# Kernel tuning notes

Hardware: AMD Instinct MI355X
Metric: run time of the kernel (lower is better)

## Reference

```python
import jax, jax.numpy as jnp
import numpy as np

B, N, L, D, H, NLAYERS, V = 8, 1024, 16, 256, 4, 2, 32000
DH = D // H  # per-head dim


def setup_inputs() -> dict:
    key = jax.random.key(0)
    ks = jax.random.split(key, 7)
    cfg_adj = jax.random.randint(ks[0], (B, N, N), 0, 2, dtype=jnp.int32)
    cfg_nodes = jax.random.randint(ks[1], (B, N, L), 0, V, dtype=jnp.int32)
    cfg_len = jax.random.randint(ks[2], (B,), 1, N + 1, dtype=jnp.int32)
    emb = jax.random.normal(ks[3], (V, D), jnp.float32) * 0.02
    # xavier-ish scale for per-head projections and attention vectors
    W = jax.random.normal(ks[4], (NLAYERS, H, D, DH), jnp.float32) * np.float32(np.sqrt(2.0 / (D + DH)))
    a_src = jax.random.normal(ks[5], (NLAYERS, H, DH), jnp.float32) * 0.1
    a_dst = jax.random.normal(ks[6], (NLAYERS, H, DH), jnp.float32) * 0.1
    ln_scale = jnp.ones((NLAYERS, D), jnp.float32)
    ln_bias = jnp.zeros((NLAYERS, D), jnp.float32)
    return {"cfg_adj": cfg_adj, "cfg_nodes": cfg_nodes, "cfg_len": cfg_len,
            "emb": emb, "W": W, "a_src": a_src, "a_dst": a_dst,
            "ln_scale": ln_scale, "ln_bias": ln_bias}


def _layer_norm(x, scale, bias, eps=1e-5):
    mu = jnp.mean(x, axis=-1, keepdims=True)
    var = jnp.var(x, axis=-1, keepdims=True)
    return (x - mu) * jax.lax.rsqrt(var + eps) * scale + bias


def reference(cfg_adj, cfg_nodes, cfg_len, emb, W, a_src, a_dst, ln_scale, ln_bias):
    # node features: mean over token embeddings (dropout is identity in eval)
    node_feat = emb[cfg_nodes].mean(axis=2)                       # (B,N,D)
    # add self-loops once (repeated add+clamp in the original is idempotent)
    adj = jnp.minimum(cfg_adj + jnp.eye(N, dtype=cfg_adj.dtype)[None], 1)
    neg_mask = (adj == 0)[:, None]                                # (B,1,N,N)
    h = node_feat
    for l in range(NLAYERS):
        Wh = jnp.einsum('bnd,hdk->bhnk', h, W[l])                 # (B,H,N,DH)
        src = jnp.einsum('bhnk,hk->bhn', Wh, a_src[l])            # (B,H,N)
        dst = jnp.einsum('bhnk,hk->bhn', Wh, a_dst[l])            # (B,H,N)
        e = jax.nn.leaky_relu(src[:, :, :, None] + dst[:, :, None, :], 0.2)
        e = jnp.where(neg_mask, jnp.float32(-1e9), e)             # masked fill
        alpha = jax.nn.softmax(e, axis=-1)                        # (B,H,N,N)
        h_prime = jnp.einsum('bhnm,bhmk->bhnk', alpha, Wh)        # (B,H,N,DH)
        h_cat = jnp.transpose(h_prime, (0, 2, 1, 3)).reshape(B, N, D)
        h = _layer_norm(h + h_cat, ln_scale[l], ln_bias[l])
    return h, cfg_len
```

## Files before the change

kernel.cpp:

```cpp
#include <hip/hip_runtime.h>
#include <math.h>

#define B 8
#define N 1024
#define L 16
#define D 256
#define H 4
#define DH 64
#define NLAYERS 2
#define V 32000

typedef __attribute__((ext_vector_type(8))) short short8;
typedef __attribute__((ext_vector_type(4))) float f32x4;

union U8 { uint4 u; short8 s; };

__device__ inline unsigned short f2bf(float x) {
    unsigned u = __float_as_uint(x);
    u = (u + 0x7fff + ((u >> 16) & 1)) >> 16;
    return (unsigned short)u;
}
__device__ inline float bf2f(unsigned short x) {
    return __uint_as_float(((unsigned)x) << 16);
}


#define PACK_BLK 2048
#define WT_BLK   (NLAYERS * H * 4)
#define PRE_GRID (PACK_BLK + WT_BLK + 1)

__global__ __launch_bounds__(256) void k_pre(const int* __restrict__ adj,
                                             const float* __restrict__ W,
                                             const int* __restrict__ len,
                                             unsigned long long* __restrict__ pack,
                                             unsigned short* __restrict__ WT_sw,
                                             float* __restrict__ out_len) {
    int bid = blockIdx.x;
    int t = threadIdx.x;
    if (bid < PACK_BLK) {
        int row = bid * 4 + (t >> 6);
        int lane = t & 63;
        int n = row & (N - 1);
        const int* arow = adj + (long)row * N;
        unsigned long long* prow = pack + (size_t)row * 16;
        int g16 = lane & 15;
#pragma unroll
        for (int it = 0; it < 4; ++it) {
            int m0 = it * 256 + lane * 4;
            int4 a = *(const int4*)(arow + m0);
            unsigned nib = (unsigned)((a.x != 0) || (m0 == n))
                         | ((unsigned)((a.y != 0) || (m0 + 1 == n)) << 1)
                         | ((unsigned)((a.z != 0) || (m0 + 2 == n)) << 2)
                         | ((unsigned)((a.w != 0) || (m0 + 3 == n)) << 3);
            unsigned long long v = (unsigned long long)nib << (g16 * 4);
            v |= __shfl_xor(v, 1, 64);
            v |= __shfl_xor(v, 2, 64);
            v |= __shfl_xor(v, 4, 64);
            v |= __shfl_xor(v, 8, 64);
            if (g16 == 0) prow[it * 4 + (lane >> 4)] = v;
        }
    } else if (bid < PACK_BLK + WT_BLK) {
        int idx = bid - PACK_BLK;
        int lh = idx >> 2, q = idx & 3;
        const float* Wl = W + (size_t)lh * D * DH;
        int dh = t & 63;
        int d0 = q * 64 + (t >> 6) * 16;
#pragma unroll
        for (int i = 0; i < 16; ++i) {
            int d = d0 + i;
            WT_sw[(((size_t)lh * 8 + (d >> 5)) * 64 + dh) * 32 + (d & 31)] = f2bf(Wl[(size_t)d * DH + dh]);
        }
    } else {
        if (t < B) out_len[t] = (float)len[t];
    }
}

__device__ inline void wh_tile(const unsigned short* __restrict__ hA,
                               const unsigned short* __restrict__ WT_l,
                               const float* __restrict__ asrc_l,
                               const float* __restrict__ adst_l,
                               unsigned short* __restrict__ WhT_out,
                               float* __restrict__ srcv_out,
                               float* __restrict__ dstv_out,
                               int b, int n0, int hh, int lane) {
    int rowLane = lane & 15, quad = lane >> 4;
    int bh = b * H + hh;
    const unsigned short* abase = hA + rowLane * 32 + quad * 8;
    const unsigned short* bbase = WT_l + (size_t)hh * 16384 + rowLane * 32 + quad * 8;
    f32x4 acc[4] = {};
#pragma unroll
    for (int kc = 0; kc < 8; ++kc) {
        short8 af = *(const short8*)(abase + kc * 512);
#pragma unroll
        for (int c = 0; c < 4; ++c) {
            short8 bf = *(const short8*)(bbase + (size_t)kc * 2048 + c * 512);
            acc[c] = __builtin_amdgcn_mfma_f32_16x16x32_bf16(af, bf, acc[c], 0, 0, 0);
        }
    }
    int m0 = n0 + quad * 4;
    float ps[4] = {0.f, 0.f, 0.f, 0.f}, pd[4] = {0.f, 0.f, 0.f, 0.f};
#pragma unroll
    for (int c = 0; c < 4; ++c) {
        int dh = c * 16 + rowLane;
        ushort4 o;
        o.x = f2bf(acc[c][0]); o.y = f2bf(acc[c][1]);
        o.z = f2bf(acc[c][2]); o.w = f2bf(acc[c][3]);
        *(ushort4*)&WhT_out[(((size_t)bh * 32 + (m0 >> 5)) * 64 + dh) * 32 + (m0 & 31)] = o;
        float as = asrc_l[hh * DH + dh];
        float ad = adst_l[hh * DH + dh];
#pragma unroll
        for (int r = 0; r < 4; ++r) { ps[r] += acc[c][r] * as; pd[r] += acc[c][r] * ad; }
    }
#pragma unroll
    for (int off = 1; off < 16; off <<= 1) {
#pragma unroll
        for (int r = 0; r < 4; ++r) {
            ps[r] += __shfl_xor(ps[r], off, 64);
            pd[r] += __shfl_xor(pd[r], off, 64);
        }
    }
    if (rowLane == 0) {
#pragma unroll
        for (int r = 0; r < 4; ++r) {
            srcv_out[bh * N + m0 + r] = ps[r];
            dstv_out[bh * N + m0 + r] = pd[r];
        }
    }
}

__global__ __launch_bounds__(1024) void k_feat(const float* __restrict__ emb,
                                               const int* __restrict__ nodes,
                                               unsigned short* __restrict__ h_sw,
                                               const unsigned short* __restrict__ WT0,
                                               const float* __restrict__ asrc0,
                                               const float* __restrict__ adst0,
                                               unsigned short* __restrict__ WhT0,
                                               float* __restrict__ srcv0,
                                               float* __restrict__ dstv0) {
    __shared__ __align__(16) int nodesLds[256];
    __shared__ __align__(16) unsigned short hA[8 * 16 * 32];
    int tid = threadIdx.x;
    int bt = blockIdx.x;
    int b = bt >> 6, nt = bt & 63, n0 = nt * 16;
    if (tid < 256) nodesLds[tid] = nodes[(size_t)(b * N + n0) * L + tid];
    __syncthreads();
    int w = tid >> 6, lane = tid & 63;
    int d4 = lane * 4;
    const int* np = nodesLds + w * L;
    float4 s = make_float4(0.f, 0.f, 0.f, 0.f);
#pragma unroll
    for (int l = 0; l < L; ++l) {
        float4 v = *(const float4*)&emb[(size_t)np[l] * D + d4];
        s.x += v.x; s.y += v.y; s.z += v.z; s.w += v.w;
    }
    s.x *= (1.0f / L); s.y *= (1.0f / L); s.z *= (1.0f / L); s.w *= (1.0f / L);
    ushort4 o;
    o.x = f2bf(s.x); o.y = f2bf(s.y); o.z = f2bf(s.z); o.w = f2bf(s.w);
    int off = (d4 >> 5) * 512 + w * 32 + (d4 & 31);
    *(ushort4*)&hA[off] = o;
    *(ushort4*)&h_sw[((size_t)(b * 64 + nt) * 8) * 512 + off] = o;
    __syncthreads();
    if (w < 4) wh_tile(hA, WT0, asrc0, adst0, WhT0, srcv0, dstv0, b, n0, w, lane);
}

template <int FINAL>
__global__ __launch_bounds__(256) void k_attn_f(const unsigned long long* __restrict__ pack,
                                                const float* __restrict__ srcv_in,
                                                const float* __restrict__ dstv_in,
                                                const unsigned short* __restrict__ WhT_in,
                                                unsigned short* __restrict__ h_sw,
                                                const float* __restrict__ scale_l,
                                                const float* __restrict__ bias_l,
                                                const unsigned short* __restrict__ WT_next,
                                                const float* __restrict__ asrc_n,
                                                const float* __restrict__ adst_n,
                                                unsigned short* __restrict__ WhT_out,
                                                float* __restrict__ srcv_out,
                                                float* __restrict__ dstv_out,
                                                float* __restrict__ out) {
    __shared__ __align__(16) char smem[25600];
    float* dsts = (float*)smem;
    unsigned long long* packs = (unsigned long long*)(smem + 16384);
    float* xt = (float*)smem;
    unsigned short* hA = (unsigned short*)(smem + 17408);

    int tid = threadIdx.x;
    int bt = blockIdx.x;
    int b = bt >> 6, nt = bt & 63, n0 = nt * 16;
    int w = tid >> 6, lane = tid & 63;
    int rowLane = lane & 15, quad = lane >> 4;
    int bh = b * H + w;

    {
        const float* dv = dstv_in + (size_t)bh * N;
#pragma unroll
        for (int k = 0; k < 4; ++k)
            *(float4*)(dsts + w * 1024 + k * 256 + lane * 4) = *(const float4*)(dv + k * 256 + lane * 4);
        packs[tid] = pack[((size_t)(b * N + n0 + (tid >> 4))) * 16 + (tid & 15)];
    }
    __syncthreads();

    float src = srcv_in[bh * N + n0 + rowLane];
    float mx = src > 0.f ? src : 0.2f * src;
    const unsigned* prow = (const unsigned*)packs + rowLane * 32;
    const unsigned short* wbase = WhT_in + (size_t)bh * 65536 + rowLane * 32 + quad * 8;
    const float* dw = dsts + w * 1024 + quad * 8;

    f32x4 acc[4] = {};
    float sum0 = 0.f, sum1 = 0.f;
    short8 fb[2][4];
#pragma unroll
    for (int c = 0; c < 4; ++c) fb[0][c] = *(const short8*)(wbase + c * 512);
#pragma unroll 2
    for (int t2 = 0; t2 < 32; ++t2) {
        int cb = t2 & 1;
        int t2n = (t2 + 1) & 31;
#pragma unroll
        for (int c = 0; c < 4; ++c)
            fb[cb ^ 1][c] = *(const short8*)(wbase + (size_t)t2n * 2048 + c * 512);
        unsigned bits = (prow[t2] >> (quad * 8)) & 0xffu;
        float4 d0 = *(const float4*)(dw + t2 * 32);
        float4 d1 = *(const float4*)(dw + t2 * 32 + 4);
        float dd[8] = {d0.x, d0.y, d0.z, d0.w, d1.x, d1.y, d1.z, d1.w};
        unsigned pk[4];
#pragma unroll
        for (int j2 = 0; j2 < 4; ++j2) {
            float ea = src + dd[2 * j2];
            float eb = src + dd[2 * j2 + 1];
            ea = ea > 0.f ? ea : 0.2f * ea;
            eb = eb > 0.f ? eb : 0.2f * eb;
            float pa = ((bits >> (2 * j2)) & 1) ? __expf(ea - mx) : 0.f;
            float pb = ((bits >> (2 * j2 + 1)) & 1) ? __expf(eb - mx) : 0.f;
            sum0 += pa; sum1 += pb;
            pk[j2] = (__float_as_uint(pb) & 0xffff0000u) | (__float_as_uint(pa) >> 16);
        }
        U8 u; u.u = make_uint4(pk[0], pk[1], pk[2], pk[3]);
        short8 af = u.s;
        acc[0] = __builtin_amdgcn_mfma_f32_16x16x32_bf16(af, fb[cb][0], acc[0], 0, 0, 0);
        acc[1] = __builtin_amdgcn_mfma_f32_16x16x32_bf16(af, fb[cb][1], acc[1], 0, 0, 0);
        acc[2] = __builtin_amdgcn_mfma_f32_16x16x32_bf16(af, fb[cb][2], acc[2], 0, 0, 0);
        acc[3] = __builtin_amdgcn_mfma_f32_16x16x32_bf16(af, fb[cb][3], acc[3], 0, 0, 0);
    }
    float sum = sum0 + sum1;
    sum += __shfl_xor(sum, 16, 64);
    sum += __shfl_xor(sum, 32, 64);
    float inv[4];
#pragma unroll
    for (int r = 0; r < 4; ++r) inv[r] = 1.0f / __shfl(sum, quad * 4 + r, 64);

    __syncthreads();
#pragma unroll
    for (int c = 0; c < 4; ++c)
#pragma unroll
        for (int r = 0; r < 4; ++r)
            xt[(quad * 4 + r) * 268 + w * 64 + c * 16 + rowLane] = acc[c][r] * inv[r];
    __syncthreads();

    int row = tid >> 4, g = tid & 15;
    size_t hsb = ((size_t)(b * 64 + nt) * 8 + (g >> 1)) * 512 + row * 32 + (g & 1) * 16;
    U8 r0, r1;
    r0.u = *(const uint4*)(h_sw + hsb);
    r1.u = *(const uint4*)(h_sw + hsb + 8);
    float4 xr[4];
#pragma unroll
    for (int k = 0; k < 4; ++k) xr[k] = *(const float4*)(xt + row * 268 + g * 16 + k * 4);
    float xv[16];
    float s = 0.f, s2 = 0.f;
#pragma unroll
    for (int j = 0; j < 16; ++j) {
        unsigned short hv = (j < 8) ? ((const unsigned short*)&r0)[j] : ((const unsigned short*)&r1)[j - 8];
        float x = bf2f(hv) + ((const float*)xr)[j];
        xv[j] = x; s += x; s2 += x * x;
    }
#pragma unroll
    for (int off = 1; off < 16; off <<= 1) {
        s += __shfl_xor(s, off, 64);
        s2 += __shfl_xor(s2, off, 64);
    }
    float mu = s * (1.0f / D);
    float var = s2 * (1.0f / D) - mu * mu;
    float rstd = rsqrtf(var + 1e-5f);
    int d0 = g * 16;
    if (FINAL) {
        float* orow = out + ((size_t)(b * N) + n0 + row) * D + d0;
#pragma unroll
        for (int k = 0; k < 4; ++k) {
            float4 sc = *(const float4*)(scale_l + d0 + k * 4);
            float4 bi = *(const float4*)(bias_l + d0 + k * 4);
            float4 y;
            y.x = (xv[k * 4 + 0] - mu) * rstd * sc.x + bi.x;
            y.y = (xv[k * 4 + 1] - mu) * rstd * sc.y + bi.y;
            y.z = (xv[k * 4 + 2] - mu) * rstd * sc.z + bi.z;
            y.w = (xv[k * 4 + 3] - mu) * rstd * sc.w + bi.w;
            *(float4*)(orow + k * 4) = y;
        }
    } else {
        U8 o0, o1;
#pragma unroll
        for (int j = 0; j < 16; ++j) {
            float scv = scale_l[d0 + j];
            float biv = bias_l[d0 + j];
            unsigned short yb = f2bf((xv[j] - mu) * rstd * scv + biv);
            if (j < 8) ((unsigned short*)&o0)[j] = yb;
            else ((unsigned short*)&o1)[j - 8] = yb;
        }
        *(uint4*)(h_sw + hsb) = o0.u;
        *(uint4*)(h_sw + hsb + 8) = o1.u;
        unsigned short* ha = hA + (g >> 1) * 512 + row * 32 + (g & 1) * 16;
        *(uint4*)ha = o0.u;
        *(uint4*)(ha + 8) = o1.u;
        __syncthreads();
        wh_tile(hA, WT_next, asrc_n, adst_n, WhT_out, srcv_out, dstv_out, b, n0, w, lane);
    }
}

extern "C" void kernel_launch(void* const* d_in, const int* in_sizes, int n_in,
                              void* d_out, int out_size, void* d_ws, size_t ws_size,
                              hipStream_t stream) {
    const int* cfg_adj = (const int*)d_in[0];
    const int* cfg_nodes = (const int*)d_in[1];
    const int* cfg_len = (const int*)d_in[2];
    const float* emb = (const float*)d_in[3];
    const float* W = (const float*)d_in[4];
    const float* a_src = (const float*)d_in[5];
    const float* a_dst = (const float*)d_in[6];
    const float* ln_scale = (const float*)d_in[7];
    const float* ln_bias = (const float*)d_in[8];
    float* out = (float*)d_out;
    float* ws = (float*)d_ws;

    float* srcv0 = ws;
    float* dstv0 = srcv0 + (size_t)B * H * N;
    float* srcv1 = dstv0 + (size_t)B * H * N;
    float* dstv1 = srcv1 + (size_t)B * H * N;
    unsigned short* h_sw = (unsigned short*)(dstv1 + (size_t)B * H * N);
    unsigned short* WhT0 = h_sw + (size_t)B * N * D;
    unsigned short* WhT1 = WhT0 + (size_t)B * H * DH * N;
    unsigned short* WT_sw = WhT1 + (size_t)B * H * DH * N;
    unsigned long long* pack = (unsigned long long*)(WT_sw + (size_t)NLAYERS * H * DH * D);

    k_pre<<<PRE_GRID, 256, 0, stream>>>(cfg_adj, W, cfg_len, pack, WT_sw, out + (size_t)B * N * D);
    k_feat<<<B * 64, 1024, 0, stream>>>(emb, cfg_nodes, h_sw, WT_sw, a_src, a_dst,
                                        WhT0, srcv0, dstv0);
    k_attn_f<0><<<B * 64, 256, 0, stream>>>(pack, srcv0, dstv0, WhT0, h_sw,
                                            ln_scale, ln_bias,
                                            WT_sw + (size_t)H * DH * D,
                                            a_src + (size_t)H * DH, a_dst + (size_t)H * DH,
                                            WhT1, srcv1, dstv1, nullptr);
    k_attn_f<1><<<B * 64, 256, 0, stream>>>(pack, srcv1, dstv1, WhT1, h_sw,
                                            ln_scale + D, ln_bias + D,
                                            nullptr, nullptr, nullptr,
                                            nullptr, nullptr, nullptr, out);
}
```

Measured before the change: 173.5 us.

## Split attention key range across two wave halves and co-schedule adjacency packing with features

The attention kernel moves from 256 to 512 threads. Two groups of four waves each handle half of the key dimension for the same rows, and their partial outputs and softmax sums are combined through shared memory before layer norm. Adjacency bit-packing moves out of the pre-kernel into the feature kernel as extra blocks, so the small weight-transpose kernel runs alone first. This aims to raise parallelism and latency hiding in the attention loop, at the cost of more shared memory and an extra reduction.

Result: no change. 176.7 us (+1.8%).

```diff
diff --git a/kernel.cpp b/kernel.cpp
--- a/kernel.cpp
+++ b/kernel.cpp
@@ -25,24 +25,98 @@
 }
 
 
-#define PACK_BLK 2048
-#define WT_BLK   (NLAYERS * H * 4)
-#define PRE_GRID (PACK_BLK + WT_BLK + 1)
-
-__global__ __launch_bounds__(256) void k_pre(const int* __restrict__ adj,
-                                             const float* __restrict__ W,
-                                             const int* __restrict__ len,
+__global__ __launch_bounds__(1024) void k_pre(const float* __restrict__ W,
+                                              const int* __restrict__ len,
+                                              unsigned short* __restrict__ WT_sw,
+                                              float* __restrict__ out_len) {
+    int bt = blockIdx.x, tid = threadIdx.x;
+    if (bt < NLAYERS * H) {
+        int lh = bt;
+        const float* Wl = W + (size_t)lh * D * DH;
+        int dh = tid & 63;
+        int d0 = (tid >> 6) * 16;
+#pragma unroll
+        for (int i = 0; i < 16; ++i) {
+            int d = d0 + i;
+            WT_sw[(((size_t)lh * 8 + (d >> 5)) * 64 + dh) * 32 + (d & 31)] = f2bf(Wl[(size_t)d * DH + dh]);
+        }
+    } else {
+        if (tid < B) out_len[tid] = (float)len[tid];
+    }
+}
+
+__device__ inline void wh_tile(const unsigned short* hA_t,
+                               const unsigned short* __restrict__ WT_l,
+                               const float* __restrict__ asrc_l,
+                               const float* __restrict__ adst_l,
+                               unsigned short* __restrict__ WhT_out,
+                               float* __restrict__ srcv_out,
+                               float* __restrict__ dstv_out,
+                               int b, int n0t, int hh, int lane) {
+    int rowLane = lane & 15, quad = lane >> 4;
+    int bh = b * H + hh;
+    const unsigned short* abase = hA_t + rowLane * 32 + quad * 8;
+    const unsigned short* bbase = WT_l + (size_t)hh * 16384 + rowLane * 32 + quad * 8;
+    f32x4 acc[4] = {};
+#pragma unroll
+    for (int kc = 0; kc < 8; ++kc) {
+        short8 af = *(const short8*)(abase + kc * 512);
+#pragma unroll
+        for (int c = 0; c < 4; ++c) {
+            short8 bf = *(const short8*)(bbase + (size_t)kc * 2048 + c * 512);
+            acc[c] = __builtin_amdgcn_mfma_f32_16x16x32_bf16(af, bf, acc[c], 0, 0, 0);
+        }
+    }
+    int m0 = n0t + quad * 4;
+    float ps[4] = {0.f, 0.f, 0.f, 0.f}, pd[4] = {0.f, 0.f, 0.f, 0.f};
+#pragma unroll
+    for (int c = 0; c < 4; ++c) {
+        int dh = c * 16 + rowLane;
+        ushort4 o;
+        o.x = f2bf(acc[c][0]); o.y = f2bf(acc[c][1]);
+        o.z = f2bf(acc[c][2]); o.w = f2bf(acc[c][3]);
+        *(ushort4*)&WhT_out[(((size_t)bh * 32 + (m0 >> 5)) * 64 + dh) * 32 + (m0 & 31)] = o;
+        float as = asrc_l[hh * DH + dh];
+        float ad = adst_l[hh * DH + dh];
+#pragma unroll
+        for (int r = 0; r < 4; ++r) { ps[r] += acc[c][r] * as; pd[r] += acc[c][r] * ad; }
+    }
+#pragma unroll
+    for (int off = 1; off < 16; off <<= 1) {
+#pragma unroll
+        for (int r = 0; r < 4; ++r) {
+            ps[r] += __shfl_xor(ps[r], off, 64);
+            pd[r] += __shfl_xor(pd[r], off, 64);
+        }
+    }
+    if (rowLane == 0) {
+#pragma unroll
+        for (int r = 0; r < 4; ++r) {
+            srcv_out[bh * N + m0 + r] = ps[r];
+            dstv_out[bh * N + m0 + r] = pd[r];
+        }
+    }
+}
+
+__global__ __launch_bounds__(1024) void k_gp(const float* __restrict__ emb,
+                                             const int* __restrict__ nodes,
+                                             const int* __restrict__ adj,
+                                             unsigned short* __restrict__ h_sw,
                                              unsigned long long* __restrict__ pack,
-                                             unsigned short* __restrict__ WT_sw,
-                                             float* __restrict__ out_len) {
-    int bid = blockIdx.x;
-    int t = threadIdx.x;
-    if (bid < PACK_BLK) {
-        int row = bid * 4 + (t >> 6);
-        int lane = t & 63;
-        int n = row & (N - 1);
-        const int* arow = adj + (long)row * N;
-        unsigned long long* prow = pack + (size_t)row * 16;
+                                             const unsigned short* __restrict__ WT0,
+                                             const float* __restrict__ asrc0,
+                                             const float* __restrict__ adst0,
+                                             unsigned short* __restrict__ WhT0,
+                                             float* __restrict__ srcv0,
+                                             float* __restrict__ dstv0) {
+    int bt = blockIdx.x, tid = threadIdx.x;
+    int wg = tid >> 6, lane = tid & 63;
+    if (bt >= 512) {
+        int idx = bt - 512;
+        int b = idx >> 6, n0 = (idx & 63) * 16;
+        int n = n0 + wg;
+        const int* arow = adj + ((size_t)(b * N + n)) * N;
+        unsigned long long* prow = pack + ((size_t)(b * N + n)) * 16;
         int g16 = lane & 15;
 #pragma unroll
         for (int it = 0; it < 4; ++it) {
@@ -59,165 +133,95 @@
             v |= __shfl_xor(v, 8, 64);
             if (g16 == 0) prow[it * 4 + (lane >> 4)] = v;
         }
-    } else if (bid < PACK_BLK + WT_BLK) {
-        int idx = bid - PACK_BLK;
-        int lh = idx >> 2, q = idx & 3;
-        const float* Wl = W + (size_t)lh * D * DH;
-        int dh = t & 63;
-        int d0 = q * 64 + (t >> 6) * 16;
-#pragma unroll
-        for (int i = 0; i < 16; ++i) {
-            int d = d0 + i;
-            WT_sw[(((size_t)lh * 8 + (d >> 5)) * 64 + dh) * 32 + (d & 31)] = f2bf(Wl[(size_t)d * DH + dh]);
-        }
-    } else {
-        if (t < B) out_len[t] = (float)len[t];
-    }
-}
-
-__device__ inline void wh_tile(const unsigned short* __restrict__ hA,
-                               const unsigned short* __restrict__ WT_l,
-                               const float* __restrict__ asrc_l,
-                               const float* __restrict__ adst_l,
-                               unsigned short* __restrict__ WhT_out,
-                               float* __restrict__ srcv_out,
-                               float* __restrict__ dstv_out,
-                               int b, int n0, int hh, int lane) {
-    int rowLane = lane & 15, quad = lane >> 4;
-    int bh = b * H + hh;
-    const unsigned short* abase = hA + rowLane * 32 + quad * 8;
-    const unsigned short* bbase = WT_l + (size_t)hh * 16384 + rowLane * 32 + quad * 8;
-    f32x4 acc[4] = {};
-#pragma unroll
-    for (int kc = 0; kc < 8; ++kc) {
-        short8 af = *(const short8*)(abase + kc * 512);
-#pragma unroll
-        for (int c = 0; c < 4; ++c) {
-            short8 bf = *(const short8*)(bbase + (size_t)kc * 2048 + c * 512);
-            acc[c] = __builtin_amdgcn_mfma_f32_16x16x32_bf16(af, bf, acc[c], 0, 0, 0);
-        }
-    }
-    int m0 = n0 + quad * 4;
-    float ps[4] = {0.f, 0.f, 0.f, 0.f}, pd[4] = {0.f, 0.f, 0.f, 0.f};
-#pragma unroll
-    for (int c = 0; c < 4; ++c) {
-        int dh = c * 16 + rowLane;
-        ushort4 o;
-        o.x = f2bf(acc[c][0]); o.y = f2bf(acc[c][1]);
-        o.z = f2bf(acc[c][2]); o.w = f2bf(acc[c][3]);
-        *(ushort4*)&WhT_out[(((size_t)bh * 32 + (m0 >> 5)) * 64 + dh) * 32 + (m0 & 31)] = o;
-        float as = asrc_l[hh * DH + dh];
-        float ad = adst_l[hh * DH + dh];
-#pragma unroll
-        for (int r = 0; r < 4; ++r) { ps[r] += acc[c][r] * as; pd[r] += acc[c][r] * ad; }
-    }
-#pragma unroll
-    for (int off = 1; off < 16; off <<= 1) {
-#pragma unroll
-        for (int r = 0; r < 4; ++r) {
-            ps[r] += __shfl_xor(ps[r], off, 64);
-            pd[r] += __shfl_xor(pd[r], off, 64);
-        }
-    }
-    if (rowLane == 0) {
-#pragma unroll
-        for (int r = 0; r < 4; ++r) {
-            srcv_out[bh * N + m0 + r] = ps[r];
-            dstv_out[bh * N + m0 + r] = pd[r];
-        }
-    }
-}
-
-__global__ __launch_bounds__(1024) void k_feat(const float* __restrict__ emb,
-                                               const int* __restrict__ nodes,
-                                               unsigned short* __restrict__ h_sw,
-                                               const unsigned short* __restrict__ WT0,
-                                               const float* __restrict__ asrc0,
-                                               const float* __restrict__ adst0,
-                                               unsigned short* __restrict__ WhT0,
-                                               float* __restrict__ srcv0,
-                                               float* __restrict__ dstv0) {
+        return;
+    }
     __shared__ __align__(16) int nodesLds[256];
     __shared__ __align__(16) unsigned short hA[8 * 16 * 32];
+    int b = bt >> 6, nt = bt & 63, n0 = nt * 16;
+    if (tid < 256) nodesLds[tid] = nodes[((size_t)(b * N + n0)) * L + tid];
+    __syncthreads();
+    int d4 = lane * 4;
+    const int* np = nodesLds + wg * L;
+    float4 s = make_float4(0.f, 0.f, 0.f, 0.f);
+#pragma unroll
+    for (int l = 0; l < L; ++l) {
+        float4 v = *(const float4*)&emb[(size_t)np[l] * D + d4];
+        s.x += v.x; s.y += v.y; s.z += v.z; s.w += v.w;
+    }
+    s.x *= (1.0f / L); s.y *= (1.0f / L); s.z *= (1.0f / L); s.w *= (1.0f / L);
+    ushort4 o;
+    o.x = f2bf(s.x); o.y = f2bf(s.y); o.z = f2bf(s.z); o.w = f2bf(s.w);
+    int off = (d4 >> 5) * 512 + wg * 32 + (d4 & 31);
+    *(ushort4*)&hA[off] = o;
+    *(ushort4*)&h_sw[((size_t)(b * 64 + nt) * 8) * 512 + off] = o;
+    __syncthreads();
+    if (wg < 4) wh_tile(hA, WT0, asrc0, adst0, WhT0, srcv0, dstv0, b, n0, wg, lane);
+}
+
+#define AT_XT1  17408
+#define AT_PACK 34560
+#define AT_HA   36608
+#define AT_SSUM 44800
+#define AT_SIZE 45312
+
+template <int FINAL>
+__global__ __launch_bounds__(512, 4) void k_attn2(const unsigned long long* __restrict__ pack,
+                                                  const float* __restrict__ srcv_in,
+                                                  const float* __restrict__ dstv_in,
+                                                  const unsigned short* __restrict__ WhT_in,
+                                                  unsigned short* __restrict__ h_sw,
+                                                  const float* __restrict__ scale_l,
+                                                  const float* __restrict__ bias_l,
+                                                  const unsigned short* __restrict__ WT_next,
+                                                  const float* __restrict__ asrc_n,
+                                                  const float* __restrict__ adst_n,
+                                                  unsigned short* __restrict__ WhT_out,
+                                                  float* __restrict__ srcv_out,
+                                                  float* __restrict__ dstv_out,
+                                                  float* __restrict__ out) {
+    __shared__ __align__(16) char smem[AT_SIZE];
+    float* dsts = (float*)smem;
+    float* xt0 = (float*)smem;
+    float* xt1 = (float*)(smem + AT_XT1);
+    unsigned long long* packs = (unsigned long long*)(smem + AT_PACK);
+    unsigned short* hA = (unsigned short*)(smem + AT_HA);
+    float* ssum = (float*)(smem + AT_SSUM);
+
     int tid = threadIdx.x;
     int bt = blockIdx.x;
     int b = bt >> 6, nt = bt & 63, n0 = nt * 16;
-    if (tid < 256) nodesLds[tid] = nodes[(size_t)(b * N + n0) * L + tid];
-    __syncthreads();
-    int w = tid >> 6, lane = tid & 63;
-    int d4 = lane * 4;
-    const int* np = nodesLds + w * L;
-    float4 s = make_float4(0.f, 0.f, 0.f, 0.f);
-#pragma unroll
-    for (int l = 0; l < L; ++l) {
-        float4 v = *(const float4*)&emb[(size_t)np[l] * D + d4];
-        s.x += v.x; s.y += v.y; s.z += v.z; s.w += v.w;
-    }
-    s.x *= (1.0f / L); s.y *= (1.0f / L); s.z *= (1.0f / L); s.w *= (1.0f / L);
-    ushort4 o;
-    o.x = f2bf(s.x); o.y = f2bf(s.y); o.z = f2bf(s.z); o.w = f2bf(s.w);
-    int off = (d4 >> 5) * 512 + w * 32 + (d4 & 31);
-    *(ushort4*)&hA[off] = o;
-    *(ushort4*)&h_sw[((size_t)(b * 64 + nt) * 8) * 512 + off] = o;
-    __syncthreads();
-    if (w < 4) wh_tile(hA, WT0, asrc0, adst0, WhT0, srcv0, dstv0, b, n0, w, lane);
-}
-
-template <int FINAL>
-__global__ __launch_bounds__(256) void k_attn_f(const unsigned long long* __restrict__ pack,
-                                                const float* __restrict__ srcv_in,
-                                                const float* __restrict__ dstv_in,
-                                                const unsigned short* __restrict__ WhT_in,
-                                                unsigned short* __restrict__ h_sw,
-                                                const float* __restrict__ scale_l,
-                                                const float* __restrict__ bias_l,
-                                                const unsigned short* __restrict__ WT_next,
-                                                const float* __restrict__ asrc_n,
-                                                const float* __restrict__ adst_n,
-                                                unsigned short* __restrict__ WhT_out,
-                                                float* __restrict__ srcv_out,
-                                                float* __restrict__ dstv_out,
-                                                float* __restrict__ out) {
-    __shared__ __align__(16) char smem[25600];
-    float* dsts = (float*)smem;
-    unsigned long long* packs = (unsigned long long*)(smem + 16384);
-    float* xt = (float*)smem;
-    unsigned short* hA = (unsigned short*)(smem + 17408);
-
-    int tid = threadIdx.x;
-    int bt = blockIdx.x;
-    int b = bt >> 6, nt = bt & 63, n0 = nt * 16;
-    int w = tid >> 6, lane = tid & 63;
+    int wg = tid >> 6, lane = tid & 63;
+    int half = wg >> 2, hh = wg & 3;
     int rowLane = lane & 15, quad = lane >> 4;
-    int bh = b * H + w;
+    int bh = b * H + hh;
 
     {
-        const float* dv = dstv_in + (size_t)bh * N;
-#pragma unroll
-        for (int k = 0; k < 4; ++k)
-            *(float4*)(dsts + w * 1024 + k * 256 + lane * 4) = *(const float4*)(dv + k * 256 + lane * 4);
-        packs[tid] = pack[((size_t)(b * N + n0 + (tid >> 4))) * 16 + (tid & 15)];
+        const float* dv = dstv_in + (size_t)bh * N + half * 512;
+        *(float4*)(dsts + hh * 1024 + half * 512 + lane * 4) = *(const float4*)(dv + lane * 4);
+        *(float4*)(dsts + hh * 1024 + half * 512 + 256 + lane * 4) = *(const float4*)(dv + 256 + lane * 4);
+        if (tid < 256) packs[tid] = pack[((size_t)(b * N + n0 + (tid >> 4))) * 16 + (tid & 15)];
     }
     __syncthreads();
 
     float src = srcv_in[bh * N + n0 + rowLane];
     float mx = src > 0.f ? src : 0.2f * src;
-    const unsigned* prow = (const unsigned*)packs + rowLane * 32;
+    const unsigned* prow = (const unsigned*)packs + rowLane * 32 + half * 16;
     const unsigned short* wbase = WhT_in + (size_t)bh * 65536 + rowLane * 32 + quad * 8;
-    const float* dw = dsts + w * 1024 + quad * 8;
+    const float* dw = dsts + hh * 1024 + half * 512 + quad * 8;
 
     f32x4 acc[4] = {};
     float sum0 = 0.f, sum1 = 0.f;
     short8 fb[2][4];
 #pragma unroll
-    for (int c = 0; c < 4; ++c) fb[0][c] = *(const short8*)(wbase + c * 512);
+    for (int c = 0; c < 4; ++c)
+        fb[0][c] = *(const short8*)(wbase + (size_t)(half * 16) * 2048 + c * 512);
 #pragma unroll 2
-    for (int t2 = 0; t2 < 32; ++t2) {
+    for (int t2 = 0; t2 < 16; ++t2) {
         int cb = t2 & 1;
-        int t2n = (t2 + 1) & 31;
+        int t2n = (t2 + 1) & 15;
 #pragma unroll
         for (int c = 0; c < 4; ++c)
-            fb[cb ^ 1][c] = *(const short8*)(wbase + (size_t)t2n * 2048 + c * 512);
+            fb[cb ^ 1][c] = *(const short8*)(wbase + (size_t)(half * 16 + t2n) * 2048 + c * 512);
         unsigned bits = (prow[t2] >> (quad * 8)) & 0xffu;
         float4 d0 = *(const float4*)(dw + t2 * 32);
         float4 d1 = *(const float4*)(dw + t2 * 32 + 4);
@@ -244,49 +248,55 @@
     float sum = sum0 + sum1;
     sum += __shfl_xor(sum, 16, 64);
     sum += __shfl_xor(sum, 32, 64);
+    if (quad == 0) ssum[wg * 16 + rowLane] = sum;
+    __syncthreads();
+
     float inv[4];
 #pragma unroll
-    for (int r = 0; r < 4; ++r) inv[r] = 1.0f / __shfl(sum, quad * 4 + r, 64);
-
-    __syncthreads();
+    for (int r = 0; r < 4; ++r) {
+        int rr = quad * 4 + r;
+        inv[r] = 1.0f / (ssum[hh * 16 + rr] + ssum[(4 + hh) * 16 + rr]);
+    }
+    float* xtw = half ? xt1 : xt0;
 #pragma unroll
     for (int c = 0; c < 4; ++c)
 #pragma unroll
         for (int r = 0; r < 4; ++r)
-            xt[(quad * 4 + r) * 268 + w * 64 + c * 16 + rowLane] = acc[c][r] * inv[r];
-    __syncthreads();
-
-    int row = tid >> 4, g = tid & 15;
-    size_t hsb = ((size_t)(b * 64 + nt) * 8 + (g >> 1)) * 512 + row * 32 + (g & 1) * 16;
-    U8 r0, r1;
+            xtw[(quad * 4 + r) * 268 + hh * 64 + c * 16 + rowLane] = acc[c][r] * inv[r];
+    __syncthreads();
+
+    int row = tid >> 5, c8 = tid & 31;
+    int d0c = c8 * 8;
+    size_t hsb = ((size_t)(b * 64 + nt) * 8 + (c8 >> 2)) * 512 + row * 32 + (c8 & 3) * 8;
+    U8 r0;
     r0.u = *(const uint4*)(h_sw + hsb);
-    r1.u = *(const uint4*)(h_sw + hsb + 8);
-    float4 xr[4];
-#pragma unroll
-    for (int k = 0; k < 4; ++k) xr[k] = *(const float4*)(xt + row * 268 + g * 16 + k * 4);
-    float xv[16];
+    float4 xa0 = *(const float4*)(xt0 + row * 268 + d0c);
+    float4 xa1 = *(const float4*)(xt0 + row * 268 + d0c + 4);
+    float4 xb0 = *(const float4*)(xt1 + row * 268 + d0c);
+    float4 xb1 = *(const float4*)(xt1 + row * 268 + d0c + 4);
+    float xp[8] = {xa0.x + xb0.x, xa0.y + xb0.y, xa0.z + xb0.z, xa0.w + xb0.w,
+                   xa1.x + xb1.x, xa1.y + xb1.y, xa1.z + xb1.z, xa1.w + xb1.w};
+    float xv[8];
     float s = 0.f, s2 = 0.f;
 #pragma unroll
-    for (int j = 0; j < 16; ++j) {
-        unsigned short hv = (j < 8) ? ((const unsigned short*)&r0)[j] : ((const unsigned short*)&r1)[j - 8];
-        float x = bf2f(hv) + ((const float*)xr)[j];
+    for (int j = 0; j < 8; ++j) {
+        float x = bf2f(((const unsigned short*)&r0)[j]) + xp[j];
         xv[j] = x; s += x; s2 += x * x;
     }
 #pragma unroll
-    for (int off = 1; off < 16; off <<= 1) {
-        s += __shfl_xor(s, off, 64);
-        s2 += __shfl_xor(s2, off, 64);
+    for (int off = 1; off < 32; off <<= 1) {
+        s += __shfl_xor(s, off, 32);
+        s2 += __shfl_xor(s2, off, 32);
     }
     float mu = s * (1.0f / D);
     float var = s2 * (1.0f / D) - mu * mu;
     float rstd = rsqrtf(var + 1e-5f);
-    int d0 = g * 16;
     if (FINAL) {
-        float* orow = out + ((size_t)(b * N) + n0 + row) * D + d0;
-#pragma unroll
-        for (int k = 0; k < 4; ++k) {
-            float4 sc = *(const float4*)(scale_l + d0 + k * 4);
-            float4 bi = *(const float4*)(bias_l + d0 + k * 4);
+        float* orow = out + ((size_t)(b * N) + n0 + row) * D + d0c;
+#pragma unroll
+        for (int k = 0; k < 2; ++k) {
+            float4 sc = *(const float4*)(scale_l + d0c + k * 4);
+            float4 bi = *(const float4*)(bias_l + d0c + k * 4);
             float4 y;
             y.x = (xv[k * 4 + 0] - mu) * rstd * sc.x + bi.x;
             y.y = (xv[k * 4 + 1] - mu) * rstd * sc.y + bi.y;
@@ -295,22 +305,18 @@
             *(float4*)(orow + k * 4) = y;
         }
     } else {
-        U8 o0, o1;
-#pragma unroll
-        for (int j = 0; j < 16; ++j) {
-            float scv = scale_l[d0 + j];
-            float biv = bias_l[d0 + j];
-            unsigned short yb = f2bf((xv[j] - mu) * rstd * scv + biv);
-            if (j < 8) ((unsigned short*)&o0)[j] = yb;
-            else ((unsigned short*)&o1)[j - 8] = yb;
+        U8 o0;
+#pragma unroll
+        for (int j = 0; j < 8; ++j) {
+            float scv = scale_l[d0c + j];
+            float biv = bias_l[d0c + j];
+            ((unsigned short*)&o0)[j] = f2bf((xv[j] - mu) * rstd * scv + biv);
         }
         *(uint4*)(h_sw + hsb) = o0.u;
-        *(uint4*)(h_sw + hsb + 8) = o1.u;
-        unsigned short* ha = hA + (g >> 1) * 512 + row * 32 + (g & 1) * 16;
-        *(uint4*)ha = o0.u;
-        *(uint4*)(ha + 8) = o1.u;
+        *(uint4*)&hA[(c8 >> 2) * 512 + row * 32 + (c8 & 3) * 8] = o0.u;
         __syncthreads();
-        wh_tile(hA, WT_next, asrc_n, adst_n, WhT_out, srcv_out, dstv_out, b, n0, w, lane);
+        if (wg < 4)
+            wh_tile(hA, WT_next, asrc_n, adst_n, WhT_out, srcv_out, dstv_out, b, n0, wg, lane);
     }
 }
 
@@ -337,18 +343,18 @@
     unsigned short* WhT0 = h_sw + (size_t)B * N * D;
     unsigned short* WhT1 = WhT0 + (size_t)B * H * DH * N;
     unsigned short* WT_sw = WhT1 + (size_t)B * H * DH * N;
-    unsigned long long* pack = (unsigned long long*)(WT_sw + (size_t)NLAYERS * H * DH * D);
-
-    k_pre<<<PRE_GRID, 256, 0, stream>>>(cfg_adj, W, cfg_len, pack, WT_sw, out + (size_t)B * N * D);
-    k_feat<<<B * 64, 1024, 0, stream>>>(emb, cfg_nodes, h_sw, WT_sw, a_src, a_dst,
-                                        WhT0, srcv0, dstv0);
-    k_attn_f<0><<<B * 64, 256, 0, stream>>>(pack, srcv0, dstv0, WhT0, h_sw,
-                                            ln_scale, ln_bias,
-                                            WT_sw + (size_t)H * DH * D,
-                                            a_src + (size_t)H * DH, a_dst + (size_t)H * DH,
-                                            WhT1, srcv1, dstv1, nullptr);
-    k_attn_f<1><<<B * 64, 256, 0, stream>>>(pack, srcv1, dstv1, WhT1, h_sw,
-                                            ln_scale + D, ln_bias + D,
-                                            nullptr, nullptr, nullptr,
-                                            nullptr, nullptr, nullptr, out);
-}
+    unsigned long long* pack = (unsigned long long*)(WT_sw + (size_t)NLAYERS * H * D * DH);
+
+    k_pre<<<NLAYERS * H + 1, 1024, 0, stream>>>(W, cfg_len, WT_sw, out + (size_t)B * N * D);
+    k_gp<<<1024, 1024, 0, stream>>>(emb, cfg_nodes, cfg_adj, h_sw, pack,
+                                    WT_sw, a_src, a_dst, WhT0, srcv0, dstv0);
+    k_attn2<0><<<512, 512, 0, stream>>>(pack, srcv0, dstv0, WhT0, h_sw,
+                                        ln_scale, ln_bias,
+                                        WT_sw + (size_t)H * 16384,
+                                        a_src + (size_t)H * DH, a_dst + (size_t)H * DH,
+                                        WhT1, srcv1, dstv1, nullptr);
+    k_attn2<1><<<512, 512, 0, stream>>>(pack, srcv1, dstv1, WhT1, h_sw,
+                                        ln_scale + D, ln_bias + D,
+                                        nullptr, nullptr, nullptr,
+                                        nullptr, nullptr, nullptr, out);
+}
```
